# Kernel tuning notes

Hardware: AMD Instinct MI355X
Metric: run time of the kernel (lower is better)

The kernel has to match this reference:

```python
import math
import jax, jax.numpy as jnp
import numpy as np

B, T, D = 4, 2048, 1024
H, DH = 16, 64
FF = 4096
EPS = 1e-5


def setup_inputs() -> dict:
    key = jax.random.key(0)
    ks = jax.random.split(key, 12)
    s = 0.02
    inp = {
        "x": jax.random.normal(ks[0], (B, T, D), dtype=jnp.float32),
        "ln1_g": jnp.ones((D,), jnp.float32),
        "ln1_b": jnp.zeros((D,), jnp.float32),
        "ln2_g": jnp.ones((D,), jnp.float32),
        "ln2_b": jnp.zeros((D,), jnp.float32),
        # torch nn.Linear convention: weight shape [out, in], y = x @ W.T + b
        "wq": jax.random.normal(ks[1], (D, D), jnp.float32) * s,
        "bq": jnp.zeros((D,), jnp.float32),
        "wk": jax.random.normal(ks[2], (D, D), jnp.float32) * s,
        "bk": jnp.zeros((D,), jnp.float32),
        "wv": jax.random.normal(ks[3], (D, D), jnp.float32) * s,
        "bv": jnp.zeros((D,), jnp.float32),
        "wo": jax.random.normal(ks[4], (D, D), jnp.float32) * s,
        "bo": jnp.zeros((D,), jnp.float32),
        "w1": jax.random.normal(ks[5], (FF, D), jnp.float32) * s,
        "b1": jnp.zeros((FF,), jnp.float32),
        "w2": jax.random.normal(ks[6], (D, FF), jnp.float32) * s,
        "b2": jnp.zeros((D,), jnp.float32),
    }
    return inp


def _layernorm(h, g, b):
    mu = jnp.mean(h, axis=-1, keepdims=True)
    var = jnp.mean(jnp.square(h - mu), axis=-1, keepdims=True)
    return (h - mu) * jax.lax.rsqrt(var + EPS) * g + b


def _block(x, ln1_g, ln1_b, ln2_g, ln2_b, wq, bq, wk, bk, wv, bv, wo, bo, w1, b1, w2, b2):
    b, t, d = x.shape
    h = _layernorm(x, ln1_g, ln1_b)
    q = (h @ wq.T + bq).reshape(b, t, H, DH)
    k = (h @ wk.T + bk).reshape(b, t, H, DH)
    v = (h @ wv.T + bv).reshape(b, t, H, DH)
    # full (non-causal) attention, as in the torch module
    att = jnp.einsum("bqhd,bkhd->bhqk", q, k) / math.sqrt(DH)
    att = jax.nn.softmax(att, axis=-1)
    out = jnp.einsum("bhqk,bkhd->bqhd", att, v).reshape(b, t, d)
    x = x + (out @ wo.T + bo)
    h2 = _layernorm(x, ln2_g, ln2_b)
    ff = jax.nn.gelu(h2 @ w1.T + b1, approximate=False) @ w2.T + b2
    return x + ff


def reference(x, ln1_g, ln1_b, ln2_g, ln2_b, wq, bq, wk, bk, wv, bv, wo, bo, w1, b1, w2, b2):
    return _block(x, ln1_g, ln1_b, ln2_g, ln2_b, wq, bq, wk, bk, wv, bv, wo, bo, w1, b1, w2, b2)
```

## Files before the change

### kernel.cpp

```cpp
#include <hip/hip_runtime.h>
#include <cstdint>
#include <cstddef>

typedef __attribute__((ext_vector_type(8))) __bf16 bf16x8;
typedef __attribute__((ext_vector_type(4))) float f32x4;
typedef __attribute__((ext_vector_type(8))) unsigned short us8;
typedef __attribute__((ext_vector_type(4))) unsigned short us4;

__device__ inline unsigned short f2bf(float f) {
    unsigned int u = __float_as_uint(f);
    u += 0x7fffu + ((u >> 16) & 1u);
    return (unsigned short)(u >> 16);
}

__device__ inline unsigned int pkbf_t(float hi, float lo) {
    return __builtin_amdgcn_perm(__float_as_uint(hi), __float_as_uint(lo), 0x07060302u);
}

__device__ inline void async_copy16(const void* g, void* l) {
    __builtin_amdgcn_global_load_lds(
        (const __attribute__((address_space(1))) unsigned int*)g,
        (__attribute__((address_space(3))) unsigned int*)l, 16, 0, 0);
}

__global__ __launch_bounds__(256) void cvt_bf16(const float* __restrict__ in,
                                                unsigned short* __restrict__ out, int n4) {
    int i = blockIdx.x * 256 + threadIdx.x;
    if (i < n4) {
        float4 v = ((const float4*)in)[i];
        us4 o;
        o[0] = f2bf(v.x); o[1] = f2bf(v.y); o[2] = f2bf(v.z); o[3] = f2bf(v.w);
        ((us4*)out)[i] = o;
    }
}

__global__ __launch_bounds__(256) void ln_bf16(const float* __restrict__ X,
                                               const float* __restrict__ g,
                                               const float* __restrict__ b,
                                               unsigned short* __restrict__ out) {
    int row = blockIdx.x;
    int t = threadIdx.x;
    float4 v = ((const float4*)(X + (size_t)row * 1024))[t];
    float s  = v.x + v.y + v.z + v.w;
    float s2 = v.x * v.x + v.y * v.y + v.z * v.z + v.w * v.w;
#pragma unroll
    for (int m = 1; m < 64; m <<= 1) {
        s  += __shfl_xor(s, m, 64);
        s2 += __shfl_xor(s2, m, 64);
    }
    __shared__ float red[8];
    int w = t >> 6, l = t & 63;
    if (l == 0) { red[w] = s; red[4 + w] = s2; }
    __syncthreads();
    s  = red[0] + red[1] + red[2] + red[3];
    s2 = red[4] + red[5] + red[6] + red[7];
    float mu  = s * (1.0f / 1024.0f);
    float var = s2 * (1.0f / 1024.0f) - mu * mu;
    float rs  = rsqrtf(var + 1e-5f);
    int c = t * 4;
    float4 gv = *(const float4*)(g + c);
    float4 bv = *(const float4*)(b + c);
    us4 o;
    o[0] = f2bf((v.x - mu) * rs * gv.x + bv.x);
    o[1] = f2bf((v.y - mu) * rs * gv.y + bv.y);
    o[2] = f2bf((v.z - mu) * rs * gv.z + bv.z);
    o[3] = f2bf((v.w - mu) * rs * gv.w + bv.w);
    *(us4*)(out + (size_t)row * 1024 + c) = o;
}

#define BM 128
#define BN 128
#define BK 32

template <int EPI>
__global__ __launch_bounds__(256) void gemm_nt(const unsigned short* __restrict__ A,
                                               const unsigned short* __restrict__ B,
                                               const float* __restrict__ bias,
                                               const float* __restrict__ resid,
                                               void* __restrict__ Cout, int N, int K) {
    __shared__ __align__(16) unsigned short As[BM * BK];
    __shared__ __align__(16) unsigned short Bs[BN * BK];
    const int tid = threadIdx.x;
    const int lane = tid & 63, w = tid >> 6;
    const int quad = lane >> 4, l16 = lane & 15;
    const int wr = w >> 1, wc = w & 1;
    const size_t bm = (size_t)blockIdx.y * BM;
    const size_t bn = (size_t)blockIdx.x * BN;

    f32x4 acc[4][4];
#pragma unroll
    for (int i = 0; i < 4; i++)
#pragma unroll
        for (int j = 0; j < 4; j++) acc[i][j] = (f32x4){0.f, 0.f, 0.f, 0.f};

    for (int k0 = 0; k0 < K; k0 += BK) {
#pragma unroll
        for (int i = 0; i < 2; i++) {
            int e = (i * 256 + tid) * 8;
            int r = e >> 5, c = e & 31;
            async_copy16(A + (bm + r) * K + k0 + c, &As[e]);
            async_copy16(B + (bn + r) * K + k0 + c, &Bs[e]);
        }
        __syncthreads();
        bf16x8 af[4], bfr[4];
#pragma unroll
        for (int mt = 0; mt < 4; mt++)
            af[mt] = *(const bf16x8*)&As[(wr * 64 + mt * 16 + l16) * BK + quad * 8];
#pragma unroll
        for (int nt = 0; nt < 4; nt++)
            bfr[nt] = *(const bf16x8*)&Bs[(wc * 64 + nt * 16 + l16) * BK + quad * 8];
#pragma unroll
        for (int mt = 0; mt < 4; mt++)
#pragma unroll
            for (int nt = 0; nt < 4; nt++)
                acc[mt][nt] = __builtin_amdgcn_mfma_f32_16x16x32_bf16(af[mt], bfr[nt],
                                                                      acc[mt][nt], 0, 0, 0);
        __syncthreads();
    }

#pragma unroll
    for (int mt = 0; mt < 4; mt++) {
#pragma unroll
        for (int nt = 0; nt < 4; nt++) {
#pragma unroll
            for (int r = 0; r < 4; r++) {
                size_t row = bm + wr * 64 + mt * 16 + quad * 4 + r;
                size_t col = bn + wc * 64 + nt * 16 + l16;
                float v = acc[mt][nt][r] + bias[col];
                if (EPI == 1) {
                    v = 0.5f * v * (1.0f + erff(v * 0.70710678118654752f));
                    ((unsigned short*)Cout)[row * N + col] = f2bf(v);
                } else if (EPI == 2) {
                    ((float*)Cout)[row * N + col] = v + resid[row * N + col];
                } else if (EPI == 6) {
                    int sel = (int)(bn >> 10);
                    if (sel == 0) {
                        ((unsigned short*)Cout)[row * 1024 + col] =
                            f2bf(v * 0.18033688011112042f);
                    } else {
                        int key = (int)row & 2047;
                        int bh  = (((int)row >> 11) << 4) | (((int)col >> 6) & 15);
                        int dh  = (int)col & 63;
                        size_t addr;
                        if (sel == 1)
                            addr = 8388608 + (size_t)bh * 131072 +
                                   (size_t)(key >> 6) * 4096 + (size_t)(key & 63) * 64 +
                                   ((((dh >> 3) ^ (key & 7))) << 3) + (dh & 7);
                        else
                            addr = 16777216 + (size_t)bh * 131072 +
                                   (size_t)(key >> 6) * 4096 + (size_t)dh * 64 +
                                   (((((key >> 3) & 7) ^ (dh & 7))) << 3) + (key & 7);
                        ((unsigned short*)Cout)[addr] = f2bf(v);
                    }
                }
            }
        }
    }
}

__global__ __launch_bounds__(256) void attn_kernel(const unsigned short* __restrict__ Q,
                                                   const unsigned short* __restrict__ Kb,
                                                   const unsigned short* __restrict__ Vtb,
                                                   unsigned short* __restrict__ O) {
    const int bh   = blockIdx.x >> 4;
    const int qblk = blockIdx.x & 15;
    const int b = bh >> 4, h = bh & 15;
    const int tid = threadIdx.x, lane = tid & 63, w = tid >> 6;
    const int quad = lane >> 4, l16 = lane & 15;
    const int sw = l16 & 7;

    __shared__ __align__(16) unsigned short smem[16384];
    unsigned short* Ks  = smem;
    unsigned short* Vts = smem + 4096;
    unsigned short* Psw = smem + 8192 + w * 2048;

    const size_t qrow0 = (size_t)b * 2048 + (size_t)qblk * 128 + w * 32;
    const int hcol = h * 64;

    bf16x8 qfr[2][2];
#pragma unroll
    for (int qf = 0; qf < 2; qf++)
#pragma unroll
        for (int kp = 0; kp < 2; kp++)
            qfr[qf][kp] = *(const bf16x8*)(Q + (qrow0 + qf * 16 + l16) * 1024 +
                                           hcol + kp * 32 + quad * 8);

    f32x4 acc[4][2];
#pragma unroll
    for (int df = 0; df < 4; df++)
#pragma unroll
        for (int qf = 0; qf < 2; qf++) acc[df][qf] = (f32x4){0.f, 0.f, 0.f, 0.f};
    float l_[2] = {0.f, 0.f};

    const unsigned short* ksrc = Kb  + (size_t)bh * 131072;
    const unsigned short* vsrc = Vtb + (size_t)bh * 131072;

    for (int kt = 0; kt < 32; ++kt) {
        __syncthreads();
        const unsigned short* kg = ksrc + kt * 4096;
        const unsigned short* vg = vsrc + kt * 4096;
        async_copy16(kg + tid * 8,        &Ks[tid * 8]);
        async_copy16(kg + 2048 + tid * 8, &Ks[2048 + tid * 8]);
        async_copy16(vg + tid * 8,        &Vts[tid * 8]);
        async_copy16(vg + 2048 + tid * 8, &Vts[2048 + tid * 8]);
        __syncthreads();

        f32x4 s[4][2];
#pragma unroll
        for (int mf = 0; mf < 4; mf++)
#pragma unroll
            for (int qf = 0; qf < 2; qf++) s[mf][qf] = (f32x4){0.f, 0.f, 0.f, 0.f};
#pragma unroll
        for (int kp = 0; kp < 2; kp++) {
#pragma unroll
            for (int mf = 0; mf < 4; mf++) {
                bf16x8 kf = *(const bf16x8*)&Ks[(mf * 16 + l16) * 64 +
                                                (((kp * 4 + quad) ^ sw) << 3)];
#pragma unroll
                for (int qf = 0; qf < 2; qf++)
                    s[mf][qf] = __builtin_amdgcn_mfma_f32_16x16x32_bf16(kf, qfr[qf][kp],
                                                                        s[mf][qf], 0, 0, 0);
            }
        }

#pragma unroll
        for (int mf = 0; mf < 4; mf++)
#pragma unroll
            for (int qf = 0; qf < 2; qf++) {
                float e0 = exp2f(s[mf][qf][0]);
                float e1 = exp2f(s[mf][qf][1]);
                float e2 = exp2f(s[mf][qf][2]);
                float e3 = exp2f(s[mf][qf][3]);
                l_[qf] += (e0 + e1) + (e2 + e3);
                *(uint2*)&Psw[(qf * 16 + l16) * 64 +
                              (((mf * 2 + (quad >> 1)) ^ sw) << 3) + ((quad & 1) << 2)] =
                    make_uint2(pkbf_t(e1, e0), pkbf_t(e3, e2));
            }
        asm volatile("s_waitcnt lgkmcnt(0)" ::: "memory");

#pragma unroll
        for (int kp = 0; kp < 2; kp++) {
            bf16x8 pf[2];
#pragma unroll
            for (int qf = 0; qf < 2; qf++)
                pf[qf] = *(const bf16x8*)&Psw[(qf * 16 + l16) * 64 +
                                              (((kp * 4 + quad) ^ sw) << 3)];
#pragma unroll
            for (int df = 0; df < 4; df++) {
                bf16x8 vf = *(const bf16x8*)&Vts[(df * 16 + l16) * 64 +
                                                 (((kp * 4 + quad) ^ sw) << 3)];
#pragma unroll
                for (int qf = 0; qf < 2; qf++)
                    acc[df][qf] = __builtin_amdgcn_mfma_f32_16x16x32_bf16(vf, pf[qf],
                                                                          acc[df][qf], 0, 0, 0);
            }
        }
    }

#pragma unroll
    for (int qf = 0; qf < 2; qf++) {
        l_[qf] += __shfl_xor(l_[qf], 16, 64);
        l_[qf] += __shfl_xor(l_[qf], 32, 64);
    }

    __syncthreads();
    float inv[2] = {1.f / l_[0], 1.f / l_[1]};
    unsigned short* Ls = smem;
#pragma unroll
    for (int df = 0; df < 4; df++)
#pragma unroll
        for (int qf = 0; qf < 2; qf++)
#pragma unroll
            for (int r = 0; r < 4; r++) {
                int dh = df * 16 + quad * 4 + r;
                int q  = w * 32 + qf * 16 + l16;
                Ls[dh * 130 + q] =
                    (unsigned short)((__float_as_uint(acc[df][qf][r] * inv[qf]) + 0x8000u) >> 16);
            }
    __syncthreads();
    int q = tid >> 1, dh0 = (tid & 1) * 32;
    size_t obase = ((size_t)b * 2048 + (size_t)qblk * 128 + q) * 1024 + hcol + dh0;
#pragma unroll
    for (int c = 0; c < 4; c++) {
        us8 o;
#pragma unroll
        for (int j = 0; j < 8; j++) o[j] = Ls[(dh0 + c * 8 + j) * 130 + q];
        *(us8*)(O + obase + c * 8) = o;
    }
}

extern "C" void kernel_launch(void* const* d_in, const int* in_sizes, int n_in,
                              void* d_out, int out_size, void* d_ws, size_t ws_size,
                              hipStream_t stream) {
    const float* x     = (const float*)d_in[0];
    const float* ln1_g = (const float*)d_in[1];
    const float* ln1_b = (const float*)d_in[2];
    const float* ln2_g = (const float*)d_in[3];
    const float* ln2_b = (const float*)d_in[4];
    const float* wq = (const float*)d_in[5];
    const float* bq = (const float*)d_in[6];
    const float* wk = (const float*)d_in[7];
    const float* bk = (const float*)d_in[8];
    const float* wv = (const float*)d_in[9];
    const float* bv = (const float*)d_in[10];
    const float* wo = (const float*)d_in[11];
    const float* bo = (const float*)d_in[12];
    const float* w1 = (const float*)d_in[13];
    const float* b1 = (const float*)d_in[14];
    const float* w2 = (const float*)d_in[15];
    const float* b2 = (const float*)d_in[16];

    const size_t MB = 1u << 20;
    char* ws = (char*)d_ws;
    unsigned short* wqkvb = (unsigned short*)(ws + 0 * MB);
    unsigned short* wob  = (unsigned short*)(ws + 6 * MB);
    unsigned short* w1b  = (unsigned short*)(ws + 8 * MB);
    unsigned short* w2b  = (unsigned short*)(ws + 16 * MB);
    unsigned short* hb   = (unsigned short*)(ws + 24 * MB);
    unsigned short* qkvb = (unsigned short*)(ws + 40 * MB);
    unsigned short* qb   = qkvb;
    unsigned short* kblk = qkvb + 8388608;
    unsigned short* vtblk= qkvb + 16777216;
    float*          x1   = (float*)(ws + 56 * MB);
    unsigned short* h2b  = (unsigned short*)(ws + 40 * MB);
    unsigned short* ff1b = (unsigned short*)(ws + 88 * MB);
    float*          bqkv = (float*)(ws + 151 * MB);

    const int D = 1024, FF = 4096, Mrows = 8192;

    cvt_bf16<<<(D * D / 4 + 255) / 256, 256, 0, stream>>>(wq, wqkvb,               D * D / 4);
    cvt_bf16<<<(D * D / 4 + 255) / 256, 256, 0, stream>>>(wk, wqkvb + D * D,       D * D / 4);
    cvt_bf16<<<(D * D / 4 + 255) / 256, 256, 0, stream>>>(wv, wqkvb + 2 * D * D,   D * D / 4);
    cvt_bf16<<<(D * D / 4 + 255) / 256, 256, 0, stream>>>(wo, wob, D * D / 4);
    cvt_bf16<<<(FF * D / 4 + 255) / 256, 256, 0, stream>>>(w1, w1b, FF * D / 4);
    cvt_bf16<<<(FF * D / 4 + 255) / 256, 256, 0, stream>>>(w2, w2b, FF * D / 4);

    hipMemcpyAsync(bqkv,            bq, D * sizeof(float), hipMemcpyDeviceToDevice, stream);
    hipMemcpyAsync(bqkv + D,        bk, D * sizeof(float), hipMemcpyDeviceToDevice, stream);
    hipMemcpyAsync(bqkv + 2 * D,    bv, D * sizeof(float), hipMemcpyDeviceToDevice, stream);

    ln_bf16<<<Mrows, 256, 0, stream>>>(x, ln1_g, ln1_b, hb);

    dim3 gQKV(3 * D / BN, Mrows / BM);
    gemm_nt<6><<<gQKV, 256, 0, stream>>>(hb, wqkvb, bqkv, nullptr, qkvb, D, D);

    attn_kernel<<<1024, 256, 0, stream>>>(qb, kblk, vtblk, hb);

    dim3 gD(D / BN, Mrows / BM);
    gemm_nt<2><<<gD, 256, 0, stream>>>(hb, wob, bo, x, x1, D, D);

    ln_bf16<<<Mrows, 256, 0, stream>>>(x1, ln2_g, ln2_b, h2b);

    dim3 gFF(FF / BN, Mrows / BM);
    gemm_nt<1><<<gFF, 256, 0, stream>>>(h2b, w1b, b1, nullptr, ff1b, FF, D);

    gemm_nt<2><<<gD, 256, 0, stream>>>(ff1b, w2b, b2, x1, (float*)d_out, D, FF);
}
```

Baseline: 635.0 us.

## Double-buffer GEMM and attention tiles, enlarge blocks, swizzle LDS, remap attention blocks to XCDs

The GEMM moves to 256x128 tiles with register-staged double-buffered LDS, an XOR swizzle to avoid bank conflicts, and a lighter barrier, so the global load of the next K slice overlaps the MFMAs. The attention kernel now handles 256 queries per block with double-buffered async K/V staging. It maps blocks so each XCD works on contiguous heads and writes its output through a swizzled row-major LDS tile. The changes aim to hide load latency and raise reuse, at the cost of more registers and LDS, lower occupancy, and fewer blocks (512 for attention).

```diff
diff --git a/kernel.cpp b/kernel.cpp
--- a/kernel.cpp
+++ b/kernel.cpp
@@ -16,6 +16,8 @@
 __device__ inline unsigned int pkbf_t(float hi, float lo) {
     return __builtin_amdgcn_perm(__float_as_uint(hi), __float_as_uint(lo), 0x07060302u);
 }
+
+#define LDS_BARRIER() asm volatile("s_waitcnt lgkmcnt(0)\ns_barrier" ::: "memory")
 
 __device__ inline void async_copy16(const void* g, void* l) {
     __builtin_amdgcn_global_load_lds(
@@ -68,18 +70,22 @@
     *(us4*)(out + (size_t)row * 1024 + c) = o;
 }
 
-#define BM 128
+#define BM 256
 #define BN 128
 #define BK 32
 
+__device__ inline int swz(int r, int c) {
+    return r * 32 + ((((c >> 3) ^ (r & 3))) << 3) + (c & 7);
+}
+
 template <int EPI>
-__global__ __launch_bounds__(256) void gemm_nt(const unsigned short* __restrict__ A,
-                                               const unsigned short* __restrict__ B,
-                                               const float* __restrict__ bias,
-                                               const float* __restrict__ resid,
-                                               void* __restrict__ Cout, int N, int K) {
-    __shared__ __align__(16) unsigned short As[BM * BK];
-    __shared__ __align__(16) unsigned short Bs[BN * BK];
+__global__ __launch_bounds__(256, 2) void gemm_nt(const unsigned short* __restrict__ A,
+                                                  const unsigned short* __restrict__ B,
+                                                  const float* __restrict__ bias,
+                                                  const float* __restrict__ resid,
+                                                  void* __restrict__ Cout, int N, int K) {
+    __shared__ __align__(16) unsigned short As[2][BM * BK];
+    __shared__ __align__(16) unsigned short Bs[2][BN * BK];
     const int tid = threadIdx.x;
     const int lane = tid & 63, w = tid >> 6;
     const int quad = lane >> 4, l16 = lane & 15;
@@ -87,44 +93,78 @@
     const size_t bm = (size_t)blockIdx.y * BM;
     const size_t bn = (size_t)blockIdx.x * BN;
 
-    f32x4 acc[4][4];
-#pragma unroll
-    for (int i = 0; i < 4; i++)
+    int ar[4], ac[4], aof[4];
+    int br[2], bc[2], bof[2];
+#pragma unroll
+    for (int i = 0; i < 4; i++) {
+        int e = (i * 256 + tid) * 8;
+        ar[i] = e >> 5; ac[i] = e & 31; aof[i] = swz(ar[i], ac[i]);
+    }
+#pragma unroll
+    for (int i = 0; i < 2; i++) {
+        int e = (i * 256 + tid) * 8;
+        br[i] = e >> 5; bc[i] = e & 31; bof[i] = swz(br[i], bc[i]);
+    }
+
+    us8 pa[4], pb[2];
+    auto ldg = [&](int k0) {
+#pragma unroll
+        for (int i = 0; i < 4; i++) pa[i] = *(const us8*)(A + (bm + ar[i]) * K + k0 + ac[i]);
+#pragma unroll
+        for (int i = 0; i < 2; i++) pb[i] = *(const us8*)(B + (bn + br[i]) * K + k0 + bc[i]);
+    };
+    auto sts = [&](int buf) {
+#pragma unroll
+        for (int i = 0; i < 4; i++) *(us8*)&As[buf][aof[i]] = pa[i];
+#pragma unroll
+        for (int i = 0; i < 2; i++) *(us8*)&Bs[buf][bof[i]] = pb[i];
+    };
+
+    f32x4 acc[8][4];
+#pragma unroll
+    for (int i = 0; i < 8; i++)
 #pragma unroll
         for (int j = 0; j < 4; j++) acc[i][j] = (f32x4){0.f, 0.f, 0.f, 0.f};
 
-    for (int k0 = 0; k0 < K; k0 += BK) {
-#pragma unroll
-        for (int i = 0; i < 2; i++) {
-            int e = (i * 256 + tid) * 8;
-            int r = e >> 5, c = e & 31;
-            async_copy16(A + (bm + r) * K + k0 + c, &As[e]);
-            async_copy16(B + (bn + r) * K + k0 + c, &Bs[e]);
-        }
-        __syncthreads();
-        bf16x8 af[4], bfr[4];
-#pragma unroll
-        for (int mt = 0; mt < 4; mt++)
-            af[mt] = *(const bf16x8*)&As[(wr * 64 + mt * 16 + l16) * BK + quad * 8];
-#pragma unroll
-        for (int nt = 0; nt < 4; nt++)
-            bfr[nt] = *(const bf16x8*)&Bs[(wc * 64 + nt * 16 + l16) * BK + quad * 8];
-#pragma unroll
-        for (int mt = 0; mt < 4; mt++)
+    ldg(0);
+    sts(0);
+    ldg(BK);
+    LDS_BARRIER();
+
+    const int nk = K / BK;
+    for (int kt = 0; kt < nk; ++kt) {
+        const int cur = kt & 1;
+        bf16x8 af[8], bfr[4];
+#pragma unroll
+        for (int mt = 0; mt < 8; mt++) {
+            int r = wr * 128 + mt * 16 + l16;
+            af[mt] = *(const bf16x8*)&As[cur][r * 32 + ((quad ^ (r & 3)) << 3)];
+        }
+#pragma unroll
+        for (int nt = 0; nt < 4; nt++) {
+            int r = wc * 64 + nt * 16 + l16;
+            bfr[nt] = *(const bf16x8*)&Bs[cur][r * 32 + ((quad ^ (r & 3)) << 3)];
+        }
+#pragma unroll
+        for (int mt = 0; mt < 8; mt++)
 #pragma unroll
             for (int nt = 0; nt < 4; nt++)
                 acc[mt][nt] = __builtin_amdgcn_mfma_f32_16x16x32_bf16(af[mt], bfr[nt],
                                                                       acc[mt][nt], 0, 0, 0);
-        __syncthreads();
-    }
-
-#pragma unroll
-    for (int mt = 0; mt < 4; mt++) {
+        if (kt + 1 < nk) {
+            sts(cur ^ 1);
+            if (kt + 2 < nk) ldg((kt + 2) * BK);
+        }
+        LDS_BARRIER();
+    }
+
+#pragma unroll
+    for (int mt = 0; mt < 8; mt++) {
 #pragma unroll
         for (int nt = 0; nt < 4; nt++) {
 #pragma unroll
             for (int r = 0; r < 4; r++) {
-                size_t row = bm + wr * 64 + mt * 16 + quad * 4 + r;
+                size_t row = bm + wr * 128 + mt * 16 + quad * 4 + r;
                 size_t col = bn + wc * 64 + nt * 16 + l16;
                 float v = acc[mt][nt][r] + bias[col];
                 if (EPI == 1) {
@@ -162,131 +202,133 @@
                                                    const unsigned short* __restrict__ Kb,
                                                    const unsigned short* __restrict__ Vtb,
                                                    unsigned short* __restrict__ O) {
-    const int bh   = blockIdx.x >> 4;
-    const int qblk = blockIdx.x & 15;
+    const int i = blockIdx.x;
+    const int xcd = i & 7, slot = i >> 3;
+    const int bh   = xcd * 8 + (slot >> 3);
+    const int qblk = slot & 7;
     const int b = bh >> 4, h = bh & 15;
     const int tid = threadIdx.x, lane = tid & 63, w = tid >> 6;
     const int quad = lane >> 4, l16 = lane & 15;
     const int sw = l16 & 7;
 
-    __shared__ __align__(16) unsigned short smem[16384];
-    unsigned short* Ks  = smem;
-    unsigned short* Vts = smem + 4096;
-    unsigned short* Psw = smem + 8192 + w * 2048;
-
-    const size_t qrow0 = (size_t)b * 2048 + (size_t)qblk * 128 + w * 32;
+    __shared__ __align__(16) unsigned short smem[32768];
+    unsigned short* Psw = smem + 16384 + w * 4096;
+
+    const size_t qrow0 = (size_t)b * 2048 + (size_t)qblk * 256 + w * 64;
     const int hcol = h * 64;
 
-    bf16x8 qfr[2][2];
-#pragma unroll
-    for (int qf = 0; qf < 2; qf++)
+    bf16x8 qfr[4][2];
+#pragma unroll
+    for (int qf = 0; qf < 4; qf++)
 #pragma unroll
         for (int kp = 0; kp < 2; kp++)
             qfr[qf][kp] = *(const bf16x8*)(Q + (qrow0 + qf * 16 + l16) * 1024 +
                                            hcol + kp * 32 + quad * 8);
 
-    f32x4 acc[4][2];
+    f32x4 acc[4][4];
 #pragma unroll
     for (int df = 0; df < 4; df++)
 #pragma unroll
-        for (int qf = 0; qf < 2; qf++) acc[df][qf] = (f32x4){0.f, 0.f, 0.f, 0.f};
-    float l_[2] = {0.f, 0.f};
+        for (int qf = 0; qf < 4; qf++) acc[df][qf] = (f32x4){0.f, 0.f, 0.f, 0.f};
+    float l_[4] = {0.f, 0.f, 0.f, 0.f};
 
     const unsigned short* ksrc = Kb  + (size_t)bh * 131072;
     const unsigned short* vsrc = Vtb + (size_t)bh * 131072;
 
-    for (int kt = 0; kt < 32; ++kt) {
-        __syncthreads();
+    auto stage = [&](int kt, int buf) {
         const unsigned short* kg = ksrc + kt * 4096;
         const unsigned short* vg = vsrc + kt * 4096;
-        async_copy16(kg + tid * 8,        &Ks[tid * 8]);
-        async_copy16(kg + 2048 + tid * 8, &Ks[2048 + tid * 8]);
-        async_copy16(vg + tid * 8,        &Vts[tid * 8]);
-        async_copy16(vg + 2048 + tid * 8, &Vts[2048 + tid * 8]);
-        __syncthreads();
-
-        f32x4 s[4][2];
-#pragma unroll
-        for (int mf = 0; mf < 4; mf++)
-#pragma unroll
-            for (int qf = 0; qf < 2; qf++) s[mf][qf] = (f32x4){0.f, 0.f, 0.f, 0.f};
-#pragma unroll
-        for (int kp = 0; kp < 2; kp++) {
-#pragma unroll
-            for (int mf = 0; mf < 4; mf++) {
-                bf16x8 kf = *(const bf16x8*)&Ks[(mf * 16 + l16) * 64 +
+        unsigned short* base = smem + buf * 8192;
+        async_copy16(kg + tid * 8,        base + tid * 8);
+        async_copy16(kg + 2048 + tid * 8, base + 2048 + tid * 8);
+        async_copy16(vg + tid * 8,        base + 4096 + tid * 8);
+        async_copy16(vg + 2048 + tid * 8, base + 6144 + tid * 8);
+    };
+
+    stage(0, 0);
+    __syncthreads();
+
+    for (int kt = 0; kt < 32; ++kt) {
+        const int cur = kt & 1;
+        if (kt + 1 < 32) stage(kt + 1, cur ^ 1);
+        const unsigned short* Kc = smem + cur * 8192;
+        const unsigned short* Vc = Kc + 4096;
+
+#pragma unroll
+        for (int mf = 0; mf < 4; mf++) {
+            f32x4 s[4];
+#pragma unroll
+            for (int qf = 0; qf < 4; qf++) s[qf] = (f32x4){0.f, 0.f, 0.f, 0.f};
+#pragma unroll
+            for (int kp = 0; kp < 2; kp++) {
+                bf16x8 kf = *(const bf16x8*)&Kc[(mf * 16 + l16) * 64 +
                                                 (((kp * 4 + quad) ^ sw) << 3)];
 #pragma unroll
-                for (int qf = 0; qf < 2; qf++)
-                    s[mf][qf] = __builtin_amdgcn_mfma_f32_16x16x32_bf16(kf, qfr[qf][kp],
-                                                                        s[mf][qf], 0, 0, 0);
+                for (int qf = 0; qf < 4; qf++)
+                    s[qf] = __builtin_amdgcn_mfma_f32_16x16x32_bf16(kf, qfr[qf][kp],
+                                                                    s[qf], 0, 0, 0);
             }
-        }
-
-#pragma unroll
-        for (int mf = 0; mf < 4; mf++)
-#pragma unroll
-            for (int qf = 0; qf < 2; qf++) {
-                float e0 = exp2f(s[mf][qf][0]);
-                float e1 = exp2f(s[mf][qf][1]);
-                float e2 = exp2f(s[mf][qf][2]);
-                float e3 = exp2f(s[mf][qf][3]);
+#pragma unroll
+            for (int qf = 0; qf < 4; qf++) {
+                float e0 = exp2f(s[qf][0]);
+                float e1 = exp2f(s[qf][1]);
+                float e2 = exp2f(s[qf][2]);
+                float e3 = exp2f(s[qf][3]);
                 l_[qf] += (e0 + e1) + (e2 + e3);
                 *(uint2*)&Psw[(qf * 16 + l16) * 64 +
                               (((mf * 2 + (quad >> 1)) ^ sw) << 3) + ((quad & 1) << 2)] =
                     make_uint2(pkbf_t(e1, e0), pkbf_t(e3, e2));
             }
+        }
         asm volatile("s_waitcnt lgkmcnt(0)" ::: "memory");
 
 #pragma unroll
         for (int kp = 0; kp < 2; kp++) {
-            bf16x8 pf[2];
-#pragma unroll
-            for (int qf = 0; qf < 2; qf++)
+            bf16x8 pf[4];
+#pragma unroll
+            for (int qf = 0; qf < 4; qf++)
                 pf[qf] = *(const bf16x8*)&Psw[(qf * 16 + l16) * 64 +
                                               (((kp * 4 + quad) ^ sw) << 3)];
 #pragma unroll
             for (int df = 0; df < 4; df++) {
-                bf16x8 vf = *(const bf16x8*)&Vts[(df * 16 + l16) * 64 +
-                                                 (((kp * 4 + quad) ^ sw) << 3)];
-#pragma unroll
-                for (int qf = 0; qf < 2; qf++)
+                bf16x8 vf = *(const bf16x8*)&Vc[(df * 16 + l16) * 64 +
+                                                (((kp * 4 + quad) ^ sw) << 3)];
+#pragma unroll
+                for (int qf = 0; qf < 4; qf++)
                     acc[df][qf] = __builtin_amdgcn_mfma_f32_16x16x32_bf16(vf, pf[qf],
                                                                           acc[df][qf], 0, 0, 0);
             }
         }
-    }
-
-#pragma unroll
-    for (int qf = 0; qf < 2; qf++) {
+        __syncthreads();
+    }
+
+    float inv[4];
+#pragma unroll
+    for (int qf = 0; qf < 4; qf++) {
         l_[qf] += __shfl_xor(l_[qf], 16, 64);
         l_[qf] += __shfl_xor(l_[qf], 32, 64);
-    }
-
+        inv[qf] = 1.0f / l_[qf];
+    }
+
+    unsigned short* Ls = smem;
+#pragma unroll
+    for (int df = 0; df < 4; df++)
+#pragma unroll
+        for (int qf = 0; qf < 4; qf++) {
+            int row = w * 64 + qf * 16 + l16;
+            us4 o;
+#pragma unroll
+            for (int r = 0; r < 4; r++)
+                o[r] = (unsigned short)((__float_as_uint(acc[df][qf][r] * inv[qf]) +
+                                         0x8000u) >> 16);
+            int chunk = df * 2 + (quad >> 1);
+            *(us4*)&Ls[row * 72 + ((chunk ^ (row & 7)) << 3) + ((quad & 1) << 2)] = o;
+        }
     __syncthreads();
-    float inv[2] = {1.f / l_[0], 1.f / l_[1]};
-    unsigned short* Ls = smem;
-#pragma unroll
-    for (int df = 0; df < 4; df++)
-#pragma unroll
-        for (int qf = 0; qf < 2; qf++)
-#pragma unroll
-            for (int r = 0; r < 4; r++) {
-                int dh = df * 16 + quad * 4 + r;
-                int q  = w * 32 + qf * 16 + l16;
-                Ls[dh * 130 + q] =
-                    (unsigned short)((__float_as_uint(acc[df][qf][r] * inv[qf]) + 0x8000u) >> 16);
-            }
-    __syncthreads();
-    int q = tid >> 1, dh0 = (tid & 1) * 32;
-    size_t obase = ((size_t)b * 2048 + (size_t)qblk * 128 + q) * 1024 + hcol + dh0;
-#pragma unroll
-    for (int c = 0; c < 4; c++) {
-        us8 o;
-#pragma unroll
-        for (int j = 0; j < 8; j++) o[j] = Ls[(dh0 + c * 8 + j) * 130 + q];
-        *(us8*)(O + obase + c * 8) = o;
-    }
+    size_t obase = ((size_t)b * 2048 + (size_t)qblk * 256 + tid) * 1024 + hcol;
+#pragma unroll
+    for (int c = 0; c < 8; c++)
+        *(us8*)(O + obase + c * 8) = *(const us8*)&Ls[tid * 72 + ((c ^ (tid & 7)) << 3)];
 }
 
 extern "C" void kernel_launch(void* const* d_in, const int* in_sizes, int n_in,
@@ -328,23 +370,23 @@
 
     const int D = 1024, FF = 4096, Mrows = 8192;
 
-    cvt_bf16<<<(D * D / 4 + 255) / 256, 256, 0, stream>>>(wq, wqkvb,               D * D / 4);
-    cvt_bf16<<<(D * D / 4 + 255) / 256, 256, 0, stream>>>(wk, wqkvb + D * D,       D * D / 4);
-    cvt_bf16<<<(D * D / 4 + 255) / 256, 256, 0, stream>>>(wv, wqkvb + 2 * D * D,   D * D / 4);
+    cvt_bf16<<<(D * D / 4 + 255) / 256, 256, 0, stream>>>(wq, wqkvb,             D * D / 4);
+    cvt_bf16<<<(D * D / 4 + 255) / 256, 256, 0, stream>>>(wk, wqkvb + D * D,     D * D / 4);
+    cvt_bf16<<<(D * D / 4 + 255) / 256, 256, 0, stream>>>(wv, wqkvb + 2 * D * D, D * D / 4);
     cvt_bf16<<<(D * D / 4 + 255) / 256, 256, 0, stream>>>(wo, wob, D * D / 4);
     cvt_bf16<<<(FF * D / 4 + 255) / 256, 256, 0, stream>>>(w1, w1b, FF * D / 4);
     cvt_bf16<<<(FF * D / 4 + 255) / 256, 256, 0, stream>>>(w2, w2b, FF * D / 4);
 
-    hipMemcpyAsync(bqkv,            bq, D * sizeof(float), hipMemcpyDeviceToDevice, stream);
-    hipMemcpyAsync(bqkv + D,        bk, D * sizeof(float), hipMemcpyDeviceToDevice, stream);
-    hipMemcpyAsync(bqkv + 2 * D,    bv, D * sizeof(float), hipMemcpyDeviceToDevice, stream);
+    hipMemcpyAsync(bqkv,         bq, D * sizeof(float), hipMemcpyDeviceToDevice, stream);
+    hipMemcpyAsync(bqkv + D,     bk, D * sizeof(float), hipMemcpyDeviceToDevice, stream);
+    hipMemcpyAsync(bqkv + 2 * D, bv, D * sizeof(float), hipMemcpyDeviceToDevice, stream);
 
     ln_bf16<<<Mrows, 256, 0, stream>>>(x, ln1_g, ln1_b, hb);
 
     dim3 gQKV(3 * D / BN, Mrows / BM);
     gemm_nt<6><<<gQKV, 256, 0, stream>>>(hb, wqkvb, bqkv, nullptr, qkvb, D, D);
 
-    attn_kernel<<<1024, 256, 0, stream>>>(qb, kblk, vtblk, hb);
+    attn_kernel<<<512, 256, 0, stream>>>(qb, kblk, vtblk, hb);
 
     dim3 gD(D / BN, Mrows / BM);
     gemm_nt<2><<<gD, 256, 0, stream>>>(hb, wob, bo, x, x1, D, D);
```

Result: slower. 738.0 us (+16.2%).
